# Kernel optimization log

Hardware: AMD Instinct MI355X
Metric: run time of the kernel (lower is better)

Reference implementation:

```python
import jax, jax.numpy as jnp
import numpy as np
from jax import lax

NPOINT = 1024
RADIUS = 0.2
NSAMPLE = 32
BN_EPS = 1e-5


def farthest_point_sample(xyz, npoint):
    # xyz: (B, N, 3). Deterministic start at index 0 (torch version starts at a
    # random index; the algorithm is otherwise identical).
    B, N, _ = xyz.shape

    def step(carry, _):
        distance, farthest = carry
        centroid = jnp.take_along_axis(xyz, farthest[:, None, None], axis=1)  # (B,1,3)
        d = jnp.sum((xyz - centroid) ** 2, axis=-1)  # (B,N)
        distance = jnp.minimum(distance, d)
        new_farthest = jnp.argmax(distance, axis=-1).astype(jnp.int32)
        return (distance, new_farthest), farthest

    init = (jnp.full((B, N), 1e10, xyz.dtype), jnp.zeros((B,), jnp.int32))
    _, centroids = lax.scan(step, init, None, length=npoint)  # (npoint, B)
    return centroids.T  # (B, npoint)


def batched_gather(points, idx):
    # points: (B, N, C); idx: (B, ...) -> (B, ..., C)
    return jax.vmap(lambda p, i: p[i])(points, idx)


def square_distance(src, dst):
    # src: (B,S,3), dst: (B,N,3) -> (B,S,N)
    d = -2.0 * jnp.einsum('bsc,bnc->bsn', src, dst)
    d += jnp.sum(src ** 2, -1)[:, :, None]
    d += jnp.sum(dst ** 2, -1)[:, None, :]
    return d


def query_ball_point(radius, nsample, xyz, new_xyz):
    B, N, _ = xyz.shape
    S = new_xyz.shape[1]
    sqrdists = square_distance(new_xyz, xyz)                 # (B,S,N)
    neg_d, idx = lax.top_k(-sqrdists, nsample)               # smallest nsample dists
    out_of_ball = (-neg_d) > radius ** 2                     # (B,S,nsample)
    first = idx[:, :, 0]
    # if even the nearest point is outside the ball, group the centroid itself
    first = jnp.where(out_of_ball[:, :, 0], jnp.arange(S, dtype=idx.dtype)[None, :], first)
    idx = jnp.where(out_of_ball, first[:, :, None], idx)
    return idx


def sa_forward(xyz_b3n, points_bdn, params):
    xyz = jnp.transpose(xyz_b3n, (0, 2, 1))      # (B,N,3)
    pts = jnp.transpose(points_bdn, (0, 2, 1))   # (B,N,D)
    fps_idx = farthest_point_sample(xyz, NPOINT)             # (B,S)
    new_xyz = batched_gather(xyz, fps_idx)                   # (B,S,3)
    idx = query_ball_point(RADIUS, NSAMPLE, xyz, new_xyz)    # (B,S,K)
    grouped_xyz = batched_gather(xyz, idx)                   # (B,S,K,3)
    grouped_xyz_norm = grouped_xyz - new_xyz[:, :, None, :]
    grouped_pts = batched_gather(pts, idx)                   # (B,S,K,D)
    x = jnp.concatenate([grouped_xyz_norm, grouped_pts], -1) # (B,S,K,3+D)

    for (w, b, gamma, beta) in params:
        x = jnp.einsum('bskc,oc->bsko', x, w) + b            # 1x1 conv
        mu = jnp.mean(x, axis=(0, 1, 2))
        var = jnp.var(x, axis=(0, 1, 2))                     # biased, as torch BN
        x = jax.nn.relu(gamma * (x - mu) * lax.rsqrt(var + BN_EPS) + beta)

    new_points = jnp.max(x, axis=2)                          # max over nsample K
    return (jnp.transpose(new_xyz, (0, 2, 1)),
            jnp.transpose(new_points, (0, 2, 1)),
            fps_idx)


def setup_inputs() -> dict:
    key = jax.random.key(0)
    ks = jax.random.split(key, 8)
    B, N, D = 16, 4096, 64
    xyz = jax.random.uniform(ks[0], (B, 3, N), dtype=jnp.float32)
    points = jax.random.normal(ks[1], (B, D, N), dtype=jnp.float32)
    mlp = [64, 64, 128]
    last = 3 + D  # in_channel = 67
    inp = {'xyz': xyz, 'points': points}
    for i, out in enumerate(mlp):
        inp[f'w{i}'] = jax.random.normal(ks[2 + i], (out, last), dtype=jnp.float32) * (1.0 / np.sqrt(last))
        inp[f'b{i}'] = jnp.zeros((out,), jnp.float32)
        inp[f'gamma{i}'] = jnp.ones((out,), jnp.float32)
        inp[f'beta{i}'] = jnp.zeros((out,), jnp.float32)
        last = out
    return inp


def reference(xyz, points, w0, b0, gamma0, beta0, w1, b1, gamma1, beta1, w2, b2, gamma2, beta2):
    params = [(w0, b0, gamma0, beta0), (w1, b1, gamma1, beta1), (w2, b2, gamma2, beta2)]
    return sa_forward(xyz, points, params)
```

## Files before the change

kernel.cpp:

```cpp
#include <hip/hip_runtime.h>

using f32x2  = __attribute__((ext_vector_type(2))) float;
using f32x4  = __attribute__((ext_vector_type(4))) float;
using short8 = __attribute__((ext_vector_type(8))) short;
using u64x2  = __attribute__((ext_vector_type(2))) unsigned long long;

__device__ __forceinline__ unsigned short f2bf(float f) {
  unsigned u = __builtin_bit_cast(unsigned, f);
  u = (u + 0x7FFFu + ((u >> 16) & 1u)) >> 16;
  return (unsigned short)u;
}
__device__ __forceinline__ float bf2f(unsigned short s) {
  return __builtin_bit_cast(float, ((unsigned)s) << 16);
}
__device__ __forceinline__ double u2d(unsigned long long u) {
  return __builtin_bit_cast(double, u);
}
__device__ __forceinline__ unsigned long long d2u(double d) {
  return __builtin_bit_cast(unsigned long long, d);
}
__device__ __forceinline__ unsigned cvt_pk_bf16(float lo, float hi) {
  unsigned r;
  asm("v_cvt_pk_bf16_f32 %0, %1, %2" : "=v"(r) : "v"(lo), "v"(hi));
  return r;
}

template <int CTRL>
__device__ __forceinline__ double dpp_max_f64(double best) {
  unsigned long long u = d2u(best);
  int lo32 = (int)(unsigned)u;
  int hi32 = (int)(unsigned)(u >> 32);
  int plo = __builtin_amdgcn_update_dpp(0, lo32, CTRL, 0xF, 0xF, true);
  int phi = __builtin_amdgcn_update_dpp(0, hi32, CTRL, 0xF, 0xF, true);
  unsigned long long p =
      ((unsigned long long)(unsigned)phi << 32) | (unsigned long long)(unsigned)plo;
  return fmax(best, u2d(p));
}
template <int CTRL>
__device__ __forceinline__ double dpp_min_f64(double v) {
  unsigned long long u = d2u(v);
  int lo32 = (int)(unsigned)u;
  int hi32 = (int)(unsigned)(u >> 32);
  int plo = __builtin_amdgcn_update_dpp(lo32, lo32, CTRL, 0xF, 0xF, false);
  int phi = __builtin_amdgcn_update_dpp(hi32, hi32, CTRL, 0xF, 0xF, false);
  unsigned long long p =
      ((unsigned long long)(unsigned)phi << 32) | (unsigned long long)(unsigned)plo;
  return fmin(v, u2d(p));
}

union SmemFP {
  struct {
    float4 sp4[4096];
    unsigned long long scand[2][16];
    int sfar[1024];
  } f;
  float tile[64][65];
};

__global__ __launch_bounds__(256, 1) void k_fp(const float* __restrict__ xyz,
                                               const float* __restrict__ points,
                                               float* __restrict__ out0,
                                               float* __restrict__ out2,
                                               int* __restrict__ fpsidx,
                                               float4* __restrict__ nq4,
                                               unsigned short* __restrict__ pT,
                                               float4* __restrict__ xyz4,
                                               const float* __restrict__ w0,
                                               const float* __restrict__ w1,
                                               const float* __restrict__ w2,
                                               unsigned short* __restrict__ wb0,
                                               unsigned short* __restrict__ wb1,
                                               unsigned short* __restrict__ wb2) {
  __shared__ SmemFP sm;
  int t = threadIdx.x, blk = blockIdx.x;
  if (blk >= 16) {
    int pb = blk - 16;
    if (pb == 1024) {
      for (int e = t; e < 64 * 96; e += 256) {
        int o = e / 96, k = e - o * 96;
        float v = (k < 64) ? w0[o * 67 + 3 + k] : ((k < 67) ? w0[o * 67 + (k - 64)] : 0.f);
        wb0[e] = f2bf(v);
      }
      for (int e = t; e < 4096; e += 256) wb1[e] = f2bf(w1[e]);
      for (int e = t; e < 8192; e += 256) wb2[e] = f2bf(w2[e]);
      return;
    }
    int b = pb >> 6, n0 = (pb & 63) << 6;
#pragma unroll
    for (int p = 0; p < 16; ++p) {
      int c = p * 4 + (t >> 6);
      sm.tile[c][t & 63] = points[(size_t)b * 262144 + (size_t)c * 4096 + n0 + (t & 63)];
    }
    if (t < 64) {
      int n = n0 + t;
      float x = xyz[(size_t)b * 12288 + n];
      float y = xyz[(size_t)b * 12288 + 4096 + n];
      float z = xyz[(size_t)b * 12288 + 8192 + n];
      float ps = __fadd_rn(__fadd_rn(__fmul_rn(x, x), __fmul_rn(y, y)), __fmul_rn(z, z));
      xyz4[(size_t)b * 4096 + n] = make_float4(x, y, z, ps);
    }
    __syncthreads();
    int nl = t >> 2, coff = (t & 3) * 16;
    unsigned v[8];
#pragma unroll
    for (int j = 0; j < 8; ++j)
      v[j] = cvt_pk_bf16(sm.tile[coff + 2 * j][nl], sm.tile[coff + 2 * j + 1][nl]);
    uint4* dst = reinterpret_cast<uint4*>(pT + ((size_t)b * 4096 + n0 + nl) * 64 + coff);
    dst[0] = make_uint4(v[0], v[1], v[2], v[3]);
    dst[1] = make_uint4(v[4], v[5], v[6], v[7]);
    return;
  }
  int b = blk;
  float px[16], py[16], pz[16], dist[16];
#pragma unroll
  for (int j = 0; j < 16; ++j) {
    int n = t + (j << 8);
    float x = xyz[(size_t)b * 12288 + n];
    float y = xyz[(size_t)b * 12288 + 4096 + n];
    float z = xyz[(size_t)b * 12288 + 8192 + n];
    px[j] = x; py[j] = y; pz[j] = z; dist[j] = 1e10f;
    sm.f.sp4[n] = make_float4(x, y, z, 0.f);
  }
  __syncthreads();
#pragma unroll
  for (int j = 0; j < 16; ++j) {
    asm volatile("" : "+v"(px[j]), "+v"(py[j]), "+v"(pz[j]));
  }
  unsigned nt = ~(unsigned)t;
  int far = 0;
  float cx = sm.f.sp4[0].x, cy = sm.f.sp4[0].y, cz = sm.f.sp4[0].z;
  for (int it = 0; it < 1024; ++it) {
    if (t == 0) sm.f.sfar[it] = far;
    double best0 = 0.0, best1 = 0.0;
#pragma unroll
    for (int j = 0; j < 16; ++j) {
      float dx = __fsub_rn(px[j], cx);
      float dy = __fsub_rn(py[j], cy);
      float dz = __fsub_rn(pz[j], cz);
      float d  = __fadd_rn(__fadd_rn(__fmul_rn(dx, dx), __fmul_rn(dy, dy)), __fmul_rn(dz, dz));
      float nd = fminf(dist[j], d);
      dist[j] = nd;
      unsigned long long cand =
          ((unsigned long long)__builtin_bit_cast(unsigned, nd) << 32) |
          (unsigned long long)(nt - (unsigned)(j << 8));
      if (j & 1) best1 = fmax(best1, u2d(cand));
      else       best0 = fmax(best0, u2d(cand));
    }
    double best = fmax(best0, best1);
    best = dpp_max_f64<0xB1>(best);
    best = dpp_max_f64<0x4E>(best);
    best = dpp_max_f64<0x124>(best);
    best = dpp_max_f64<0x128>(best);
    int pb = it & 1;
    if ((t & 15) == 0) sm.f.scand[pb][t >> 4] = d2u(best);
    __syncthreads();
    const u64x2* cp = reinterpret_cast<const u64x2*>(sm.f.scand[pb]);
    u64x2 q0 = cp[0], q1 = cp[1], q2 = cp[2], q3 = cp[3];
    u64x2 q4 = cp[4], q5 = cp[5], q6 = cp[6], q7 = cp[7];
    double a0 = fmax(u2d(q0[0]), u2d(q0[1]));
    double a1 = fmax(u2d(q1[0]), u2d(q1[1]));
    double a2 = fmax(u2d(q2[0]), u2d(q2[1]));
    double a3 = fmax(u2d(q3[0]), u2d(q3[1]));
    double a4 = fmax(u2d(q4[0]), u2d(q4[1]));
    double a5 = fmax(u2d(q5[0]), u2d(q5[1]));
    double a6 = fmax(u2d(q6[0]), u2d(q6[1]));
    double a7 = fmax(u2d(q7[0]), u2d(q7[1]));
    double b0 = fmax(fmax(a0, a1), fmax(a2, a3));
    double b1 = fmax(fmax(a4, a5), fmax(a6, a7));
    unsigned long long bw = d2u(fmax(b0, b1));
    int n = (int)(~(unsigned)bw) & 4095;
    far = n;
    float4 c4 = sm.f.sp4[n];
    cx = c4.x; cy = c4.y; cz = c4.z;
  }
  __syncthreads();
#pragma unroll
  for (int h = 0; h < 4; ++h) {
    int k = (h << 8) + t;
    int fr = sm.f.sfar[k];
    float4 p = sm.f.sp4[fr];
    float x = p.x, y = p.y, z = p.z;
    fpsidx[(b << 10) + k] = fr;
    out2[(b << 10) + k] = (float)fr;
    out0[(size_t)b * 3072 + k]        = x;
    out0[(size_t)b * 3072 + 1024 + k] = y;
    out0[(size_t)b * 3072 + 2048 + k] = z;
    float ps = __fadd_rn(__fadd_rn(__fmul_rn(x, x), __fmul_rn(y, y)), __fmul_rn(z, z));
    nq4[(b << 10) + k] = make_float4(x, y, z, ps);
  }
}

#define BCAP 384
__global__ __launch_bounds__(256) void k_ball(const float4* __restrict__ xyz4,
                                              const int* __restrict__ fpsidx,
                                              int* __restrict__ ballidx) {
  __shared__ __align__(16) float4 sp[4096];
  __shared__ unsigned long long spk[4][BCAP];
  const unsigned long long INVP = 0x7149F2CAFFFFFFFFull;
  int t = threadIdx.x, blk = blockIdx.x;
  int b = blk >> 6;
  for (int i = t; i < 4096; i += 256) sp[i] = xyz4[(size_t)b * 4096 + i];
  __syncthreads();
  int lane = t & 63, wid = t >> 6;
  for (int r = 0; r < 4; ++r) {
    int q = blk * 16 + r * 4 + wid;
    int qi = fpsidx[q];
    float4 Q = sp[qi];
    float qx = Q.x, qy = Q.y, qz = Q.z, qs = Q.w;
    int cnt = 0;
    for (int i = 0; i < 64; ++i) {
      int n = (i << 6) + lane;
      float4 P = sp[n];
      float dot = __fadd_rn(__fadd_rn(__fmul_rn(qx, P.x), __fmul_rn(qy, P.y)), __fmul_rn(qz, P.z));
      float d   = __fadd_rn(__fadd_rn(__fmul_rn(-2.f, dot), qs), P.w);
      bool in = (d <= 0.04f);
      unsigned long long m = __ballot(in);
      int pos = cnt + (int)__popcll(m & ((1ull << lane) - 1ull));
      if (in && pos < BCAP)
        spk[wid][pos] = ((unsigned long long)__builtin_bit_cast(unsigned, d) << 32) | (unsigned)n;
      cnt += (int)__popcll(m);
    }
    if (cnt > BCAP) cnt = BCAP;
    double c0, c1, c2, c3, c4, c5;
    {
      int s0 = lane, s1 = lane + 64, s2 = lane + 128, s3 = lane + 192, s4 = lane + 256, s5 = lane + 320;
      c0 = (s0 < cnt) ? u2d(spk[wid][s0]) : u2d(INVP);
      c1 = (s1 < cnt) ? u2d(spk[wid][s1]) : u2d(INVP);
      c2 = (s2 < cnt) ? u2d(spk[wid][s2]) : u2d(INVP);
      c3 = (s3 < cnt) ? u2d(spk[wid][s3]) : u2d(INVP);
      c4 = (s4 < cnt) ? u2d(spk[wid][s4]) : u2d(INVP);
      c5 = (s5 < cnt) ? u2d(spk[wid][s5]) : u2d(INVP);
    }
#define CE(a, b) { double mn_ = fmin(a, b), mx_ = fmax(a, b); a = mn_; b = mx_; }
    CE(c0, c1);
    CE(c1, c2); CE(c0, c1);
    CE(c2, c3); CE(c1, c2); CE(c0, c1);
    CE(c3, c4); CE(c2, c3); CE(c1, c2); CE(c0, c1);
    CE(c4, c5); CE(c3, c4); CE(c2, c3); CE(c1, c2); CE(c0, c1);
#undef CE
    int firstI = 0;
#pragma unroll 1
    for (int rr = 0; rr < 32; ++rr) {
      double h = c0;
      h = dpp_min_f64<0xB1>(h);
      h = dpp_min_f64<0x4E>(h);
      h = dpp_min_f64<0x124>(h);
      h = dpp_min_f64<0x128>(h);
      unsigned long long hu = d2u(h);
      int lo = (int)(unsigned)hu, hi = (int)(unsigned)(hu >> 32);
      unsigned long long r0 = ((unsigned long long)(unsigned)__builtin_amdgcn_readlane(hi, 0)  << 32) | (unsigned)__builtin_amdgcn_readlane(lo, 0);
      unsigned long long r1 = ((unsigned long long)(unsigned)__builtin_amdgcn_readlane(hi, 16) << 32) | (unsigned)__builtin_amdgcn_readlane(lo, 16);
      unsigned long long r2 = ((unsigned long long)(unsigned)__builtin_amdgcn_readlane(hi, 32) << 32) | (unsigned)__builtin_amdgcn_readlane(lo, 32);
      unsigned long long r3 = ((unsigned long long)(unsigned)__builtin_amdgcn_readlane(hi, 48) << 32) | (unsigned)__builtin_amdgcn_readlane(lo, 48);
      double w = fmin(fmin(u2d(r0), u2d(r1)), fmin(u2d(r2), u2d(r3)));
      unsigned long long wu = d2u(w);
      int wi = (int)(unsigned)wu;
      if (rr == 0) firstI = wi;
      int outv = (wu < INVP) ? wi : firstI;
      if (lane == 0) ballidx[(size_t)q * 32 + rr] = outv;
      if (d2u(c0) == wu) {
        c0 = c1; c1 = c2; c2 = c3; c3 = c4; c4 = c5; c5 = u2d(INVP);
      }
    }
  }
}

__global__ __launch_bounds__(256) void k_gemm1(const unsigned short* __restrict__ pT,
    const float4* __restrict__ xyz4, const float4* __restrict__ nq4,
    const int* __restrict__ bidx, const unsigned short* __restrict__ wb,
    const float* __restrict__ bia, unsigned short* __restrict__ xbuf,
    float* __restrict__ part) {
  __shared__ unsigned short A[64][104];
  __shared__ unsigned short W[64][104];
  __shared__ float sred[4][2][64];
  int t = threadIdx.x, blk = blockIdx.x;
  int b = blk >> 9;
  for (int e = t; e < 768; e += 256) {
    int o = e / 12, k8 = e - o * 12;
    *reinterpret_cast<uint4*>(&W[o][k8 * 8]) = reinterpret_cast<const uint4*>(wb)[e];
  }
  {
    int rt = t >> 2, sub = t & 3;
    int q = (blk << 1) + (rt >> 5);
    int n = bidx[(size_t)q * 32 + (rt & 31)];
    const uint4* src = reinterpret_cast<const uint4*>(pT + ((size_t)(b * 4096 + n)) * 64 + sub * 16);
    uint4 v0 = src[0], v1 = src[1];
    *reinterpret_cast<uint4*>(&A[rt][sub * 16])     = v0;
    *reinterpret_cast<uint4*>(&A[rt][sub * 16 + 8]) = v1;
    if (sub == 0) {
      float4 P = xyz4[(size_t)b * 4096 + n];
      float4 Qc = nq4[q];
      A[rt][64] = f2bf(__fsub_rn(P.x, Qc.x));
      A[rt][65] = f2bf(__fsub_rn(P.y, Qc.y));
      A[rt][66] = f2bf(__fsub_rn(P.z, Qc.z));
    } else if (sub == 1) {
#pragma unroll
      for (int k = 67; k < 96; ++k) A[rt][k] = 0;
    }
  }
  __syncthreads();
  int lane = t & 63, wid = t >> 6;
  int cl = lane & 15, rg = lane >> 4;
  int rowb = (wid << 4) + cl, ko = rg << 3;
  f32x4 acc[4] = {};
#pragma unroll
  for (int ks = 0; ks < 96; ks += 32) {
    short8 a = *reinterpret_cast<const short8*>(&A[rowb][ks + ko]);
#pragma unroll
    for (int nt = 0; nt < 4; ++nt) {
      short8 bb = *reinterpret_cast<const short8*>(&W[nt * 16 + cl][ks + ko]);
      acc[nt] = __builtin_amdgcn_mfma_f32_16x16x32_bf16(a, bb, acc[nt], 0, 0, 0);
    }
  }
#pragma unroll
  for (int nt = 0; nt < 4; ++nt) {
    int ch = nt * 16 + cl;
    float bv = bia[ch];
    float v0 = acc[nt][0] + bv, v1 = acc[nt][1] + bv, v2 = acc[nt][2] + bv, v3 = acc[nt][3] + bv;
    size_t gr = (size_t)blk * 64 + (wid << 4) + (rg << 2);
    xbuf[(gr + 0) * 64 + ch] = f2bf(v0);
    xbuf[(gr + 1) * 64 + ch] = f2bf(v1);
    xbuf[(gr + 2) * 64 + ch] = f2bf(v2);
    xbuf[(gr + 3) * 64 + ch] = f2bf(v3);
    float s1 = (v0 + v1) + (v2 + v3);
    float s2 = (v0 * v0 + v1 * v1) + (v2 * v2 + v3 * v3);
    s1 += __shfl_xor(s1, 16); s1 += __shfl_xor(s1, 32);
    s2 += __shfl_xor(s2, 16); s2 += __shfl_xor(s2, 32);
    if (rg == 0) { sred[wid][0][ch] = s1; sred[wid][1][ch] = s2; }
  }
  __syncthreads();
  if (t < 128) {
    int ch = t & 63, wh = t >> 6;
    float v = sred[0][wh][ch] + sred[1][wh][ch] + sred[2][wh][ch] + sred[3][wh][ch];
    part[(size_t)blk * 128 + ch * 2 + wh] = v;
  }
}

__global__ __launch_bounds__(256) void k_red(const float* __restrict__ part, int nblk, int nch,
    const float* __restrict__ gamma, const float* __restrict__ beta,
    float* __restrict__ scale, float* __restrict__ shift) {
  int c = blockIdx.x, t = threadIdx.x;
  int stride = 2 * nch;
  float s1 = 0.f, s2 = 0.f;
  for (int i = t; i < nblk; i += 256) {
    s1 += part[(size_t)i * stride + 2 * c];
    s2 += part[(size_t)i * stride + 2 * c + 1];
  }
  __shared__ float r1[256], r2[256];
  r1[t] = s1; r2[t] = s2;
  __syncthreads();
  for (int o = 128; o > 0; o >>= 1) {
    if (t < o) { r1[t] += r1[t + o]; r2[t] += r2[t + o]; }
    __syncthreads();
  }
  if (t == 0) {
    const float N = 524288.f;
    float mu = r1[0] / N;
    float var = r2[0] / N - mu * mu;
    float a = gamma[c] / sqrtf(var + 1e-5f);
    scale[c] = a;
    shift[c] = beta[c] - a * mu;
  }
}

__global__ __launch_bounds__(256) void k_gemm2(unsigned short* __restrict__ xbuf,
    const unsigned short* __restrict__ wb, const float* __restrict__ bia,
    const float* __restrict__ sc, const float* __restrict__ sh,
    float* __restrict__ part) {
  __shared__ unsigned short A[64][72];
  __shared__ unsigned short W[64][72];
  __shared__ float ssc[64], ssh[64];
  __shared__ float sred[4][2][64];
  int t = threadIdx.x, blk = blockIdx.x;
  if (t < 64) { ssc[t] = sc[t]; ssh[t] = sh[t]; }
  __syncthreads();
  for (int e = t; e < 512; e += 256) {
    int o = e >> 3, k8 = e & 7;
    *reinterpret_cast<uint4*>(&W[o][k8 * 8]) = reinterpret_cast<const uint4*>(wb)[e];
  }
  {
    int rt = t >> 2, sub = t & 3;
    size_t gr = (size_t)blk * 64 + rt;
    const uint4* src = reinterpret_cast<const uint4*>(xbuf + gr * 64 + sub * 16);
    uint4 v0 = src[0], v1 = src[1];
    unsigned wv[8] = {v0.x, v0.y, v0.z, v0.w, v1.x, v1.y, v1.z, v1.w};
    unsigned pk[8];
#pragma unroll
    for (int j = 0; j < 8; ++j) {
      int c = sub * 16 + 2 * j;
      float x0 = bf2f((unsigned short)(wv[j] & 0xffffu));
      float x1 = bf2f((unsigned short)(wv[j] >> 16));
      float a0 = fmaxf(0.f, ssc[c] * x0 + ssh[c]);
      float a1 = fmaxf(0.f, ssc[c + 1] * x1 + ssh[c + 1]);
      pk[j] = cvt_pk_bf16(a0, a1);
    }
    *reinterpret_cast<uint4*>(&A[rt][sub * 16])     = make_uint4(pk[0], pk[1], pk[2], pk[3]);
    *reinterpret_cast<uint4*>(&A[rt][sub * 16 + 8]) = make_uint4(pk[4], pk[5], pk[6], pk[7]);
  }
  __syncthreads();
  int lane = t & 63, wid = t >> 6;
  int cl = lane & 15, rg = lane >> 4;
  int rowb = (wid << 4) + cl, ko = rg << 3;
  f32x4 acc[4] = {};
#pragma unroll
  for (int ks = 0; ks < 64; ks += 32) {
    short8 a = *reinterpret_cast<const short8*>(&A[rowb][ks + ko]);
#pragma unroll
    for (int nt = 0; nt < 4; ++nt) {
      short8 bb = *reinterpret_cast<const short8*>(&W[nt * 16 + cl][ks + ko]);
      acc[nt] = __builtin_amdgcn_mfma_f32_16x16x32_bf16(a, bb, acc[nt], 0, 0, 0);
    }
  }
#pragma unroll
  for (int nt = 0; nt < 4; ++nt) {
    int ch = nt * 16 + cl;
    float bv = bia[ch];
    float v0 = acc[nt][0] + bv, v1 = acc[nt][1] + bv, v2 = acc[nt][2] + bv, v3 = acc[nt][3] + bv;
    size_t gr = (size_t)blk * 64 + (wid << 4) + (rg << 2);
    xbuf[(gr + 0) * 64 + ch] = f2bf(v0);
    xbuf[(gr + 1) * 64 + ch] = f2bf(v1);
    xbuf[(gr + 2) * 64 + ch] = f2bf(v2);
    xbuf[(gr + 3) * 64 + ch] = f2bf(v3);
    float s1 = (v0 + v1) + (v2 + v3);
    float s2 = (v0 * v0 + v1 * v1) + (v2 * v2 + v3 * v3);
    s1 += __shfl_xor(s1, 16); s1 += __shfl_xor(s1, 32);
    s2 += __shfl_xor(s2, 16); s2 += __shfl_xor(s2, 32);
    if (rg == 0) { sred[wid][0][ch] = s1; sred[wid][1][ch] = s2; }
  }
  __syncthreads();
  if (t < 128) {
    int ch = t & 63, wh = t >> 6;
    float v = sred[0][wh][ch] + sred[1][wh][ch] + sred[2][wh][ch] + sred[3][wh][ch];
    part[(size_t)blk * 128 + ch * 2 + wh] = v;
  }
}

__global__ __launch_bounds__(256) void k_gemm3(unsigned short* xbuf,
    const unsigned short* __restrict__ wb, const float* __restrict__ bia,
    const float* __restrict__ sc2, const float* __restrict__ sh2,
    float* __restrict__ part) {
  __shared__ unsigned short A[64][72];
  __shared__ unsigned short W[128][72];
  __shared__ float ssc[64], ssh[64];
  __shared__ float sred[4][4][128];
  int t = threadIdx.x, blk = blockIdx.x;
  if (t < 64) { ssc[t] = sc2[t]; ssh[t] = sh2[t]; }
  __syncthreads();
  for (int e = t; e < 1024; e += 256) {
    int o = e >> 3, k8 = e & 7;
    *reinterpret_cast<uint4*>(&W[o][k8 * 8]) = reinterpret_cast<const uint4*>(wb)[e];
  }
  {
    int rt = t >> 2, sub = t & 3;
    size_t gr = (size_t)blk * 64 + rt;
    const uint4* src = reinterpret_cast<const uint4*>(xbuf + gr * 64 + sub * 16);
    uint4 v0 = src[0], v1 = src[1];
    unsigned wv[8] = {v0.x, v0.y, v0.z, v0.w, v1.x, v1.y, v1.z, v1.w};
    unsigned pk[8];
#pragma unroll
    for (int j = 0; j < 8; ++j) {
      int c = sub * 16 + 2 * j;
      float x0 = bf2f((unsigned short)(wv[j] & 0xffffu));
      float x1 = bf2f((unsigned short)(wv[j] >> 16));
      float a0 = fmaxf(0.f, ssc[c] * x0 + ssh[c]);
      float a1 = fmaxf(0.f, ssc[c + 1] * x1 + ssh[c + 1]);
      pk[j] = cvt_pk_bf16(a0, a1);
    }
    *reinterpret_cast<uint4*>(&A[rt][sub * 16])     = make_uint4(pk[0], pk[1], pk[2], pk[3]);
    *reinterpret_cast<uint4*>(&A[rt][sub * 16 + 8]) = make_uint4(pk[4], pk[5], pk[6], pk[7]);
  }
  __syncthreads();
  int lane = t & 63, wid = t >> 6;
  int cl = lane & 15, rg = lane >> 4;
  int rowb = (wid << 4) + cl, ko = rg << 3;
  f32x4 acc[8] = {};
#pragma unroll
  for (int ks = 0; ks < 64; ks += 32) {
    short8 a = *reinterpret_cast<const short8*>(&A[rowb][ks + ko]);
#pragma unroll
    for (int nt = 0; nt < 8; ++nt) {
      short8 bb = *reinterpret_cast<const short8*>(&W[nt * 16 + cl][ks + ko]);
      acc[nt] = __builtin_amdgcn_mfma_f32_16x16x32_bf16(a, bb, acc[nt], 0, 0, 0);
    }
  }
#pragma unroll
  for (int nt = 0; nt < 8; ++nt) {
    int ch = nt * 16 + cl;
    float bv = bia[ch];
    float v0 = acc[nt][0] + bv, v1 = acc[nt][1] + bv, v2 = acc[nt][2] + bv, v3 = acc[nt][3] + bv;
    float s1 = (v0 + v1) + (v2 + v3);
    float s2 = (v0 * v0 + v1 * v1) + (v2 * v2 + v3 * v3);
    float mx = fmaxf(fmaxf(v0, v1), fmaxf(v2, v3));
    float mn = fminf(fminf(v0, v1), fminf(v2, v3));
    s1 += __shfl_xor(s1, 16); s1 += __shfl_xor(s1, 32);
    s2 += __shfl_xor(s2, 16); s2 += __shfl_xor(s2, 32);
    mx = fmaxf(mx, __shfl_xor(mx, 16)); mx = fmaxf(mx, __shfl_xor(mx, 32));
    mn = fminf(mn, __shfl_xor(mn, 16)); mn = fminf(mn, __shfl_xor(mn, 32));
    if (rg == 0) {
      sred[wid][0][ch] = s1; sred[wid][1][ch] = s2;
      sred[wid][2][ch] = mx; sred[wid][3][ch] = mn;
    }
  }
  __syncthreads();
  {
    int ch = t & 127, wh = t >> 7;
    part[(size_t)blk * 256 + ch * 2 + wh] =
        sred[0][wh][ch] + sred[1][wh][ch] + sred[2][wh][ch] + sred[3][wh][ch];
    float mx = fmaxf(sred[2 * wh][2][ch], sred[2 * wh + 1][2][ch]);
    float mn = fminf(sred[2 * wh][3][ch], sred[2 * wh + 1][3][ch]);
    float* mm = reinterpret_cast<float*>(xbuf) + (size_t)blk * 2048;
    mm[wh * 256 + ch]       = mx;
    mm[wh * 256 + 128 + ch] = mn;
  }
}

__global__ __launch_bounds__(256) void k_fin(const float* __restrict__ mm,
                                             const float* __restrict__ sc3,
                                             const float* __restrict__ sh3,
                                             float* __restrict__ out1) {
  __shared__ float tile[32][33];
  int t = threadIdx.x, blk = blockIdx.x;
  int b = blk >> 7, rem = blk & 127, ct = rem >> 5, st = rem & 31;
  int c0 = ct * 32, s0 = st * 32;
#pragma unroll
  for (int p = 0; p < 4; ++p) {
    int s_local = (t >> 5) + p * 8;
    int c = c0 + (t & 31);
    int q = (b << 10) + s0 + s_local;
    size_t base = (size_t)(q >> 1) * 2048 + (size_t)(q & 1) * 256;
    float mx = mm[base + c];
    float mn = mm[base + 128 + c];
    float sc = sc3[c], sh = sh3[c];
    float v = (sc >= 0.f) ? mx : mn;
    tile[t & 31][s_local] = fmaxf(0.f, sc * v + sh);
  }
  __syncthreads();
#pragma unroll
  for (int p = 0; p < 4; ++p) {
    int c = c0 + (t >> 5) + p * 8;
    int s = s0 + (t & 31);
    out1[(size_t)b * 131072 + (size_t)c * 1024 + s] = tile[(t >> 5) + p * 8][t & 31];
  }
}

extern "C" void kernel_launch(void* const* d_in, const int* in_sizes, int n_in,
                              void* d_out, int out_size, void* d_ws, size_t ws_size,
                              hipStream_t stream) {
  (void)in_sizes; (void)n_in; (void)out_size;
  const float* xyz    = (const float*)d_in[0];
  const float* points = (const float*)d_in[1];
  const float* w0  = (const float*)d_in[2];
  const float* b0  = (const float*)d_in[3];
  const float* g0  = (const float*)d_in[4];
  const float* be0 = (const float*)d_in[5];
  const float* w1  = (const float*)d_in[6];
  const float* b1  = (const float*)d_in[7];
  const float* g1  = (const float*)d_in[8];
  const float* be1 = (const float*)d_in[9];
  const float* w2  = (const float*)d_in[10];
  const float* b2  = (const float*)d_in[11];
  const float* g2  = (const float*)d_in[12];
  const float* be2 = (const float*)d_in[13];
  float* out  = (float*)d_out;
  float* out0 = out;
  float* out1 = out + 49152;
  float* out2 = out + 49152 + 2097152;
  char* ws = (char*)d_ws;
  const size_t OFF_PT    = 0;
  const size_t OFF_XYZ4  = 8388608;
  const size_t OFF_NQ4   = 9437184;
  const size_t OFF_FPS   = 9699328;
  const size_t OFF_BALL  = 9764864;
  const size_t OFF_XBUF  = 11862016;
  const size_t OFF_PART  = 78970880;
  const size_t OFF_SC    = 87359488;
  const size_t OFF_WB    = 87363584;
  const size_t NEED      = 87400448;
  if (ws_size < NEED) return;
  unsigned short* pT   = (unsigned short*)(ws + OFF_PT);
  float4* xyz4 = (float4*)(ws + OFF_XYZ4);
  float4* nq4  = (float4*)(ws + OFF_NQ4);
  int* fpsidx  = (int*)(ws + OFF_FPS);
  int* ballidx = (int*)(ws + OFF_BALL);
  unsigned short* xbuf = (unsigned short*)(ws + OFF_XBUF);
  float* part  = (float*)(ws + OFF_PART);
  float* scb   = (float*)(ws + OFF_SC);
  float *sc1 = scb, *sh1 = scb + 128, *sc2 = scb + 256, *sh2 = scb + 384,
        *sc3 = scb + 512, *sh3 = scb + 640;
  unsigned short* wb0 = (unsigned short*)(ws + OFF_WB);
  unsigned short* wb1 = wb0 + 6144;
  unsigned short* wb2 = wb1 + 4096;

  k_fp<<<1041, 256, 0, stream>>>(xyz, points, out0, out2, fpsidx, nq4,
                                 pT, xyz4, w0, w1, w2, wb0, wb1, wb2);
  k_ball<<<1024, 256, 0, stream>>>(xyz4, fpsidx, ballidx);
  k_gemm1<<<8192, 256, 0, stream>>>(pT, xyz4, nq4, ballidx, wb0, b0, xbuf, part);
  k_red<<<64, 256, 0, stream>>>(part, 8192, 64, g0, be0, sc1, sh1);
  k_gemm2<<<8192, 256, 0, stream>>>(xbuf, wb1, b1, sc1, sh1, part);
  k_red<<<64, 256, 0, stream>>>(part, 8192, 64, g1, be1, sc2, sh2);
  k_gemm3<<<8192, 256, 0, stream>>>(xbuf, wb2, b2, sc2, sh2, part);
  k_red<<<128, 256, 0, stream>>>(part, 8192, 128, g2, be2, sc3, sh3);
  k_fin<<<2048, 256, 0, stream>>>((const float*)xbuf, sc3, sh3, out1);
}
```

Before: 851.9 us.

## Fuse FPS, ball query and first GEMM into a persistent cooperative megakernel

Merges the farthest-point-sampling, data prep, ball-query and first-layer GEMM kernels into a single persistent cooperative kernel. The FPS blocks publish sampled centroids incrementally through progress flags, so ball-query and GEMM work can begin on finished centroids while FPS is still running. The goal is to hide the long serial FPS loop behind the downstream stages and to remove kernel launch boundaries. In exchange it adds spin-wait synchronisation, a flag memset and an occupancy query on every call, and it depends on all blocks being co-resident.

```diff
diff --git a/kernel.cpp b/kernel.cpp
--- a/kernel.cpp
+++ b/kernel.cpp
@@ -1,6 +1,5 @@
 #include <hip/hip_runtime.h>
 
-using f32x2  = __attribute__((ext_vector_type(2))) float;
 using f32x4  = __attribute__((ext_vector_type(4))) float;
 using short8 = __attribute__((ext_vector_type(8))) short;
 using u64x2  = __attribute__((ext_vector_type(2))) unsigned long long;
@@ -48,188 +47,104 @@
   return fmin(v, u2d(p));
 }
 
-union SmemFP {
-  struct {
-    float4 sp4[4096];
-    unsigned long long scand[2][16];
-    int sfar[1024];
-  } f;
+#define BCAP 384
+
+union __align__(16) SmemMega {
+  struct { float4 sp4[4096]; unsigned long long scand[2][16]; int sfar[1024]; } f;
   float tile[64][65];
+  struct { float4 sp[4096]; unsigned long long spk[4][BCAP]; } bq;
+  struct { unsigned short A[64][104]; unsigned short W[64][104]; float sred[4][2][64]; } g1;
 };
 
-__global__ __launch_bounds__(256, 1) void k_fp(const float* __restrict__ xyz,
-                                               const float* __restrict__ points,
-                                               float* __restrict__ out0,
-                                               float* __restrict__ out2,
-                                               int* __restrict__ fpsidx,
-                                               float4* __restrict__ nq4,
-                                               unsigned short* __restrict__ pT,
-                                               float4* __restrict__ xyz4,
-                                               const float* __restrict__ w0,
-                                               const float* __restrict__ w1,
-                                               const float* __restrict__ w2,
-                                               unsigned short* __restrict__ wb0,
-                                               unsigned short* __restrict__ wb1,
-                                               unsigned short* __restrict__ wb2) {
-  __shared__ SmemFP sm;
-  int t = threadIdx.x, blk = blockIdx.x;
-  if (blk >= 16) {
-    int pb = blk - 16;
-    if (pb == 1024) {
-      for (int e = t; e < 64 * 96; e += 256) {
-        int o = e / 96, k = e - o * 96;
-        float v = (k < 64) ? w0[o * 67 + 3 + k] : ((k < 67) ? w0[o * 67 + (k - 64)] : 0.f);
-        wb0[e] = f2bf(v);
-      }
-      for (int e = t; e < 4096; e += 256) wb1[e] = f2bf(w1[e]);
-      for (int e = t; e < 8192; e += 256) wb2[e] = f2bf(w2[e]);
-      return;
-    }
-    int b = pb >> 6, n0 = (pb & 63) << 6;
-#pragma unroll
-    for (int p = 0; p < 16; ++p) {
-      int c = p * 4 + (t >> 6);
-      sm.tile[c][t & 63] = points[(size_t)b * 262144 + (size_t)c * 4096 + n0 + (t & 63)];
-    }
-    if (t < 64) {
-      int n = n0 + t;
-      float x = xyz[(size_t)b * 12288 + n];
-      float y = xyz[(size_t)b * 12288 + 4096 + n];
-      float z = xyz[(size_t)b * 12288 + 8192 + n];
-      float ps = __fadd_rn(__fadd_rn(__fmul_rn(x, x), __fmul_rn(y, y)), __fmul_rn(z, z));
-      xyz4[(size_t)b * 4096 + n] = make_float4(x, y, z, ps);
-    }
-    __syncthreads();
-    int nl = t >> 2, coff = (t & 3) * 16;
-    unsigned v[8];
-#pragma unroll
-    for (int j = 0; j < 8; ++j)
-      v[j] = cvt_pk_bf16(sm.tile[coff + 2 * j][nl], sm.tile[coff + 2 * j + 1][nl]);
-    uint4* dst = reinterpret_cast<uint4*>(pT + ((size_t)b * 4096 + n0 + nl) * 64 + coff);
-    dst[0] = make_uint4(v[0], v[1], v[2], v[3]);
-    dst[1] = make_uint4(v[4], v[5], v[6], v[7]);
-    return;
-  }
-  int b = blk;
-  float px[16], py[16], pz[16], dist[16];
-#pragma unroll
-  for (int j = 0; j < 16; ++j) {
-    int n = t + (j << 8);
-    float x = xyz[(size_t)b * 12288 + n];
-    float y = xyz[(size_t)b * 12288 + 4096 + n];
-    float z = xyz[(size_t)b * 12288 + 8192 + n];
-    px[j] = x; py[j] = y; pz[j] = z; dist[j] = 1e10f;
-    sm.f.sp4[n] = make_float4(x, y, z, 0.f);
-  }
-  __syncthreads();
-#pragma unroll
-  for (int j = 0; j < 16; ++j) {
-    asm volatile("" : "+v"(px[j]), "+v"(py[j]), "+v"(pz[j]));
-  }
-  unsigned nt = ~(unsigned)t;
-  int far = 0;
-  float cx = sm.f.sp4[0].x, cy = sm.f.sp4[0].y, cz = sm.f.sp4[0].z;
-  for (int it = 0; it < 1024; ++it) {
-    if (t == 0) sm.f.sfar[it] = far;
-    double best0 = 0.0, best1 = 0.0;
-#pragma unroll
-    for (int j = 0; j < 16; ++j) {
-      float dx = __fsub_rn(px[j], cx);
-      float dy = __fsub_rn(py[j], cy);
-      float dz = __fsub_rn(pz[j], cz);
-      float d  = __fadd_rn(__fadd_rn(__fmul_rn(dx, dx), __fmul_rn(dy, dy)), __fmul_rn(dz, dz));
-      float nd = fminf(dist[j], d);
-      dist[j] = nd;
-      unsigned long long cand =
-          ((unsigned long long)__builtin_bit_cast(unsigned, nd) << 32) |
-          (unsigned long long)(nt - (unsigned)(j << 8));
-      if (j & 1) best1 = fmax(best1, u2d(cand));
-      else       best0 = fmax(best0, u2d(cand));
-    }
-    double best = fmax(best0, best1);
-    best = dpp_max_f64<0xB1>(best);
-    best = dpp_max_f64<0x4E>(best);
-    best = dpp_max_f64<0x124>(best);
-    best = dpp_max_f64<0x128>(best);
-    int pb = it & 1;
-    if ((t & 15) == 0) sm.f.scand[pb][t >> 4] = d2u(best);
-    __syncthreads();
-    const u64x2* cp = reinterpret_cast<const u64x2*>(sm.f.scand[pb]);
-    u64x2 q0 = cp[0], q1 = cp[1], q2 = cp[2], q3 = cp[3];
-    u64x2 q4 = cp[4], q5 = cp[5], q6 = cp[6], q7 = cp[7];
-    double a0 = fmax(u2d(q0[0]), u2d(q0[1]));
-    double a1 = fmax(u2d(q1[0]), u2d(q1[1]));
-    double a2 = fmax(u2d(q2[0]), u2d(q2[1]));
-    double a3 = fmax(u2d(q3[0]), u2d(q3[1]));
-    double a4 = fmax(u2d(q4[0]), u2d(q4[1]));
-    double a5 = fmax(u2d(q5[0]), u2d(q5[1]));
-    double a6 = fmax(u2d(q6[0]), u2d(q6[1]));
-    double a7 = fmax(u2d(q7[0]), u2d(q7[1]));
-    double b0 = fmax(fmax(a0, a1), fmax(a2, a3));
-    double b1 = fmax(fmax(a4, a5), fmax(a6, a7));
-    unsigned long long bw = d2u(fmax(b0, b1));
-    int n = (int)(~(unsigned)bw) & 4095;
-    far = n;
-    float4 c4 = sm.f.sp4[n];
-    cx = c4.x; cy = c4.y; cz = c4.z;
-  }
-  __syncthreads();
-#pragma unroll
-  for (int h = 0; h < 4; ++h) {
-    int k = (h << 8) + t;
-    int fr = sm.f.sfar[k];
-    float4 p = sm.f.sp4[fr];
-    float x = p.x, y = p.y, z = p.z;
-    fpsidx[(b << 10) + k] = fr;
-    out2[(b << 10) + k] = (float)fr;
-    out0[(size_t)b * 3072 + k]        = x;
-    out0[(size_t)b * 3072 + 1024 + k] = y;
-    out0[(size_t)b * 3072 + 2048 + k] = z;
+struct MegaP {
+  const float* xyz; const float* points;
+  float* out0; float* out2;
+  int* fpsidx; float4* nq4;
+  unsigned short* pT; float4* xyz4;
+  const float* w0; const float* w1; const float* w2;
+  unsigned short* wb0; unsigned short* wb1; unsigned short* wb2;
+  const float* b0;
+  unsigned short* xbuf; float* part;
+  int* bidx;
+  int* prog; int* prepcnt; int* wflag; int* ballprog;
+  int nc;
+};
+
+__device__ __forceinline__ void fps_publish(const MegaP& P, SmemMega& sm, int b, int k) {
+  int fr = sm.f.sfar[k];
+  float4 p = sm.f.sp4[fr];
+  P.fpsidx[(b << 10) + k] = fr;
+  P.out2[(b << 10) + k] = (float)fr;
+  P.out0[(size_t)b * 3072 + k]        = p.x;
+  P.out0[(size_t)b * 3072 + 1024 + k] = p.y;
+  P.out0[(size_t)b * 3072 + 2048 + k] = p.z;
+  float ps = __fadd_rn(__fadd_rn(__fmul_rn(p.x, p.x), __fmul_rn(p.y, p.y)), __fmul_rn(p.z, p.z));
+  P.nq4[(b << 10) + k] = make_float4(p.x, p.y, p.z, ps);
+}
+
+__device__ __forceinline__ void do_prep(int pb, SmemMega& sm, const MegaP& P) {
+  int t = threadIdx.x;
+  int b = pb >> 6, n0 = (pb & 63) << 6;
+#pragma unroll
+  for (int p = 0; p < 16; ++p) {
+    int c = p * 4 + (t >> 6);
+    sm.tile[c][t & 63] = P.points[(size_t)b * 262144 + (size_t)c * 4096 + n0 + (t & 63)];
+  }
+  if (t < 64) {
+    int n = n0 + t;
+    float x = P.xyz[(size_t)b * 12288 + n];
+    float y = P.xyz[(size_t)b * 12288 + 4096 + n];
+    float z = P.xyz[(size_t)b * 12288 + 8192 + n];
     float ps = __fadd_rn(__fadd_rn(__fmul_rn(x, x), __fmul_rn(y, y)), __fmul_rn(z, z));
-    nq4[(b << 10) + k] = make_float4(x, y, z, ps);
-  }
-}
-
-#define BCAP 384
-__global__ __launch_bounds__(256) void k_ball(const float4* __restrict__ xyz4,
-                                              const int* __restrict__ fpsidx,
-                                              int* __restrict__ ballidx) {
-  __shared__ __align__(16) float4 sp[4096];
-  __shared__ unsigned long long spk[4][BCAP];
+    P.xyz4[(size_t)b * 4096 + n] = make_float4(x, y, z, ps);
+  }
+  __syncthreads();
+  int nl = t >> 2, coff = (t & 3) * 16;
+  unsigned v[8];
+#pragma unroll
+  for (int j = 0; j < 8; ++j)
+    v[j] = cvt_pk_bf16(sm.tile[coff + 2 * j][nl], sm.tile[coff + 2 * j + 1][nl]);
+  uint4* dst = reinterpret_cast<uint4*>(P.pT + ((size_t)b * 4096 + n0 + nl) * 64 + coff);
+  dst[0] = make_uint4(v[0], v[1], v[2], v[3]);
+  dst[1] = make_uint4(v[4], v[5], v[6], v[7]);
+  __syncthreads();
+}
+
+__device__ __forceinline__ void do_ball(int w, SmemMega& sm, const MegaP& P) {
   const unsigned long long INVP = 0x7149F2CAFFFFFFFFull;
-  int t = threadIdx.x, blk = blockIdx.x;
-  int b = blk >> 6;
-  for (int i = t; i < 4096; i += 256) sp[i] = xyz4[(size_t)b * 4096 + i];
+  int t = threadIdx.x;
+  int b = w >> 6;
+  for (int i = t; i < 4096; i += 256) sm.bq.sp[i] = P.xyz4[(size_t)b * 4096 + i];
   __syncthreads();
   int lane = t & 63, wid = t >> 6;
   for (int r = 0; r < 4; ++r) {
-    int q = blk * 16 + r * 4 + wid;
-    int qi = fpsidx[q];
-    float4 Q = sp[qi];
+    int q = w * 16 + r * 4 + wid;
+    int qi = P.fpsidx[q];
+    float4 Q = sm.bq.sp[qi];
     float qx = Q.x, qy = Q.y, qz = Q.z, qs = Q.w;
     int cnt = 0;
     for (int i = 0; i < 64; ++i) {
       int n = (i << 6) + lane;
-      float4 P = sp[n];
-      float dot = __fadd_rn(__fadd_rn(__fmul_rn(qx, P.x), __fmul_rn(qy, P.y)), __fmul_rn(qz, P.z));
-      float d   = __fadd_rn(__fadd_rn(__fmul_rn(-2.f, dot), qs), P.w);
+      float4 Pp = sm.bq.sp[n];
+      float dot = __fadd_rn(__fadd_rn(__fmul_rn(qx, Pp.x), __fmul_rn(qy, Pp.y)), __fmul_rn(qz, Pp.z));
+      float d   = __fadd_rn(__fadd_rn(__fmul_rn(-2.f, dot), qs), Pp.w);
       bool in = (d <= 0.04f);
       unsigned long long m = __ballot(in);
       int pos = cnt + (int)__popcll(m & ((1ull << lane) - 1ull));
       if (in && pos < BCAP)
-        spk[wid][pos] = ((unsigned long long)__builtin_bit_cast(unsigned, d) << 32) | (unsigned)n;
+        sm.bq.spk[wid][pos] = ((unsigned long long)__builtin_bit_cast(unsigned, d) << 32) | (unsigned)n;
       cnt += (int)__popcll(m);
     }
     if (cnt > BCAP) cnt = BCAP;
     double c0, c1, c2, c3, c4, c5;
     {
       int s0 = lane, s1 = lane + 64, s2 = lane + 128, s3 = lane + 192, s4 = lane + 256, s5 = lane + 320;
-      c0 = (s0 < cnt) ? u2d(spk[wid][s0]) : u2d(INVP);
-      c1 = (s1 < cnt) ? u2d(spk[wid][s1]) : u2d(INVP);
-      c2 = (s2 < cnt) ? u2d(spk[wid][s2]) : u2d(INVP);
-      c3 = (s3 < cnt) ? u2d(spk[wid][s3]) : u2d(INVP);
-      c4 = (s4 < cnt) ? u2d(spk[wid][s4]) : u2d(INVP);
-      c5 = (s5 < cnt) ? u2d(spk[wid][s5]) : u2d(INVP);
+      c0 = (s0 < cnt) ? u2d(sm.bq.spk[wid][s0]) : u2d(INVP);
+      c1 = (s1 < cnt) ? u2d(sm.bq.spk[wid][s1]) : u2d(INVP);
+      c2 = (s2 < cnt) ? u2d(sm.bq.spk[wid][s2]) : u2d(INVP);
+      c3 = (s3 < cnt) ? u2d(sm.bq.spk[wid][s3]) : u2d(INVP);
+      c4 = (s4 < cnt) ? u2d(sm.bq.spk[wid][s4]) : u2d(INVP);
+      c5 = (s5 < cnt) ? u2d(sm.bq.spk[wid][s5]) : u2d(INVP);
     }
 #define CE(a, b) { double mn_ = fmin(a, b), mx_ = fmax(a, b); a = mn_; b = mx_; }
     CE(c0, c1);
@@ -252,50 +167,42 @@
       unsigned long long r1 = ((unsigned long long)(unsigned)__builtin_amdgcn_readlane(hi, 16) << 32) | (unsigned)__builtin_amdgcn_readlane(lo, 16);
       unsigned long long r2 = ((unsigned long long)(unsigned)__builtin_amdgcn_readlane(hi, 32) << 32) | (unsigned)__builtin_amdgcn_readlane(lo, 32);
       unsigned long long r3 = ((unsigned long long)(unsigned)__builtin_amdgcn_readlane(hi, 48) << 32) | (unsigned)__builtin_amdgcn_readlane(lo, 48);
-      double w = fmin(fmin(u2d(r0), u2d(r1)), fmin(u2d(r2), u2d(r3)));
-      unsigned long long wu = d2u(w);
+      double ww = fmin(fmin(u2d(r0), u2d(r1)), fmin(u2d(r2), u2d(r3)));
+      unsigned long long wu = d2u(ww);
       int wi = (int)(unsigned)wu;
       if (rr == 0) firstI = wi;
       int outv = (wu < INVP) ? wi : firstI;
-      if (lane == 0) ballidx[(size_t)q * 32 + rr] = outv;
-      if (d2u(c0) == wu) {
-        c0 = c1; c1 = c2; c2 = c3; c3 = c4; c4 = c5; c5 = u2d(INVP);
-      }
-    }
-  }
-}
-
-__global__ __launch_bounds__(256) void k_gemm1(const unsigned short* __restrict__ pT,
-    const float4* __restrict__ xyz4, const float4* __restrict__ nq4,
-    const int* __restrict__ bidx, const unsigned short* __restrict__ wb,
-    const float* __restrict__ bia, unsigned short* __restrict__ xbuf,
-    float* __restrict__ part) {
-  __shared__ unsigned short A[64][104];
-  __shared__ unsigned short W[64][104];
-  __shared__ float sred[4][2][64];
-  int t = threadIdx.x, blk = blockIdx.x;
-  int b = blk >> 9;
+      if (lane == 0) P.bidx[(size_t)q * 32 + rr] = outv;
+      if (d2u(c0) == wu) { c0 = c1; c1 = c2; c2 = c3; c3 = c4; c4 = c5; c5 = u2d(INVP); }
+    }
+  }
+  __syncthreads();
+}
+
+__device__ __forceinline__ void do_gemm1(int w, SmemMega& sm, const MegaP& P) {
+  int t = threadIdx.x;
+  int b = w >> 9;
   for (int e = t; e < 768; e += 256) {
     int o = e / 12, k8 = e - o * 12;
-    *reinterpret_cast<uint4*>(&W[o][k8 * 8]) = reinterpret_cast<const uint4*>(wb)[e];
+    *reinterpret_cast<uint4*>(&sm.g1.W[o][k8 * 8]) = reinterpret_cast<const uint4*>(P.wb0)[e];
   }
   {
     int rt = t >> 2, sub = t & 3;
-    int q = (blk << 1) + (rt >> 5);
-    int n = bidx[(size_t)q * 32 + (rt & 31)];
-    const uint4* src = reinterpret_cast<const uint4*>(pT + ((size_t)(b * 4096 + n)) * 64 + sub * 16);
+    int q = (w << 1) + (rt >> 5);
+    int n = P.bidx[(size_t)q * 32 + (rt & 31)];
+    const uint4* src = reinterpret_cast<const uint4*>(P.pT + ((size_t)(b * 4096 + n)) * 64 + sub * 16);
     uint4 v0 = src[0], v1 = src[1];
-    *reinterpret_cast<uint4*>(&A[rt][sub * 16])     = v0;
-    *reinterpret_cast<uint4*>(&A[rt][sub * 16 + 8]) = v1;
+    *reinterpret_cast<uint4*>(&sm.g1.A[rt][sub * 16])     = v0;
+    *reinterpret_cast<uint4*>(&sm.g1.A[rt][sub * 16 + 8]) = v1;
     if (sub == 0) {
-      float4 P = xyz4[(size_t)b * 4096 + n];
-      float4 Qc = nq4[q];
-      A[rt][64] = f2bf(__fsub_rn(P.x, Qc.x));
-      A[rt][65] = f2bf(__fsub_rn(P.y, Qc.y));
-      A[rt][66] = f2bf(__fsub_rn(P.z, Qc.z));
+      float4 Pt = P.xyz4[(size_t)b * 4096 + n];
+      float4 Qc = P.nq4[q];
+      sm.g1.A[rt][64] = f2bf(__fsub_rn(Pt.x, Qc.x));
+      sm.g1.A[rt][65] = f2bf(__fsub_rn(Pt.y, Qc.y));
+      sm.g1.A[rt][66] = f2bf(__fsub_rn(Pt.z, Qc.z));
     } else if (sub == 1) {
 #pragma unroll
-      for (int k = 67; k < 96; ++k) A[rt][k] = 0;
+      for (int k = 67; k < 96; ++k) sm.g1.A[rt][k] = 0;
     }
   }
   __syncthreads();
@@ -305,34 +212,151 @@
   f32x4 acc[4] = {};
 #pragma unroll
   for (int ks = 0; ks < 96; ks += 32) {
-    short8 a = *reinterpret_cast<const short8*>(&A[rowb][ks + ko]);
+    short8 a = *reinterpret_cast<const short8*>(&sm.g1.A[rowb][ks + ko]);
 #pragma unroll
     for (int nt = 0; nt < 4; ++nt) {
-      short8 bb = *reinterpret_cast<const short8*>(&W[nt * 16 + cl][ks + ko]);
+      short8 bb = *reinterpret_cast<const short8*>(&sm.g1.W[nt * 16 + cl][ks + ko]);
       acc[nt] = __builtin_amdgcn_mfma_f32_16x16x32_bf16(a, bb, acc[nt], 0, 0, 0);
     }
   }
 #pragma unroll
   for (int nt = 0; nt < 4; ++nt) {
     int ch = nt * 16 + cl;
-    float bv = bia[ch];
+    float bv = P.b0[ch];
     float v0 = acc[nt][0] + bv, v1 = acc[nt][1] + bv, v2 = acc[nt][2] + bv, v3 = acc[nt][3] + bv;
-    size_t gr = (size_t)blk * 64 + (wid << 4) + (rg << 2);
-    xbuf[(gr + 0) * 64 + ch] = f2bf(v0);
-    xbuf[(gr + 1) * 64 + ch] = f2bf(v1);
-    xbuf[(gr + 2) * 64 + ch] = f2bf(v2);
-    xbuf[(gr + 3) * 64 + ch] = f2bf(v3);
+    size_t gr = (size_t)w * 64 + (wid << 4) + (rg << 2);
+    P.xbuf[(gr + 0) * 64 + ch] = f2bf(v0);
+    P.xbuf[(gr + 1) * 64 + ch] = f2bf(v1);
+    P.xbuf[(gr + 2) * 64 + ch] = f2bf(v2);
+    P.xbuf[(gr + 3) * 64 + ch] = f2bf(v3);
     float s1 = (v0 + v1) + (v2 + v3);
     float s2 = (v0 * v0 + v1 * v1) + (v2 * v2 + v3 * v3);
     s1 += __shfl_xor(s1, 16); s1 += __shfl_xor(s1, 32);
     s2 += __shfl_xor(s2, 16); s2 += __shfl_xor(s2, 32);
-    if (rg == 0) { sred[wid][0][ch] = s1; sred[wid][1][ch] = s2; }
+    if (rg == 0) { sm.g1.sred[wid][0][ch] = s1; sm.g1.sred[wid][1][ch] = s2; }
   }
   __syncthreads();
   if (t < 128) {
     int ch = t & 63, wh = t >> 6;
-    float v = sred[0][wh][ch] + sred[1][wh][ch] + sred[2][wh][ch] + sred[3][wh][ch];
-    part[(size_t)blk * 128 + ch * 2 + wh] = v;
+    float v = sm.g1.sred[0][wh][ch] + sm.g1.sred[1][wh][ch] + sm.g1.sred[2][wh][ch] + sm.g1.sred[3][wh][ch];
+    P.part[(size_t)w * 128 + ch * 2 + wh] = v;
+  }
+  __syncthreads();
+}
+
+__global__ __launch_bounds__(256) void k_mega(MegaP P) {
+  __shared__ SmemMega sm;
+  int t = threadIdx.x, blk = blockIdx.x;
+  if (blk < 16) {
+    __builtin_amdgcn_s_setprio(2);
+    int b = blk;
+    float px[16], py[16], pz[16], dist[16];
+#pragma unroll
+    for (int j = 0; j < 16; ++j) {
+      int n = t + (j << 8);
+      float x = P.xyz[(size_t)b * 12288 + n];
+      float y = P.xyz[(size_t)b * 12288 + 4096 + n];
+      float z = P.xyz[(size_t)b * 12288 + 8192 + n];
+      px[j] = x; py[j] = y; pz[j] = z; dist[j] = 1e10f;
+      sm.f.sp4[n] = make_float4(x, y, z, 0.f);
+    }
+    __syncthreads();
+#pragma unroll
+    for (int j = 0; j < 16; ++j) {
+      asm volatile("" : "+v"(px[j]), "+v"(py[j]), "+v"(pz[j]));
+    }
+    unsigned nt = ~(unsigned)t;
+    int far = 0;
+    float cx = sm.f.sp4[0].x, cy = sm.f.sp4[0].y, cz = sm.f.sp4[0].z;
+    for (int it = 0; it < 1024; ++it) {
+      if (t == 0) sm.f.sfar[it] = far;
+      if ((it & 15) == 0 && it != 0 && t < 16) fps_publish(P, sm, b, it - 16 + t);
+      double best0 = 0.0, best1 = 0.0;
+#pragma unroll
+      for (int j = 0; j < 16; ++j) {
+        float dx = __fsub_rn(px[j], cx);
+        float dy = __fsub_rn(py[j], cy);
+        float dz = __fsub_rn(pz[j], cz);
+        float d  = __fadd_rn(__fadd_rn(__fmul_rn(dx, dx), __fmul_rn(dy, dy)), __fmul_rn(dz, dz));
+        float nd = fminf(dist[j], d);
+        dist[j] = nd;
+        unsigned long long cand =
+            ((unsigned long long)__builtin_bit_cast(unsigned, nd) << 32) |
+            (unsigned long long)(nt - (unsigned)(j << 8));
+        if (j & 1) best1 = fmax(best1, u2d(cand));
+        else       best0 = fmax(best0, u2d(cand));
+      }
+      double best = fmax(best0, best1);
+      best = dpp_max_f64<0xB1>(best);
+      best = dpp_max_f64<0x4E>(best);
+      best = dpp_max_f64<0x124>(best);
+      best = dpp_max_f64<0x128>(best);
+      int pb = it & 1;
+      if ((t & 15) == 0) sm.f.scand[pb][t >> 4] = d2u(best);
+      __syncthreads();
+      if ((it & 15) == 0 && it != 0 && t == 0) { __threadfence(); atomicExch(&P.prog[b], it); }
+      const u64x2* cp = reinterpret_cast<const u64x2*>(sm.f.scand[pb]);
+      u64x2 q0 = cp[0], q1 = cp[1], q2 = cp[2], q3 = cp[3];
+      u64x2 q4 = cp[4], q5 = cp[5], q6 = cp[6], q7 = cp[7];
+      double a0 = fmax(u2d(q0[0]), u2d(q0[1]));
+      double a1 = fmax(u2d(q1[0]), u2d(q1[1]));
+      double a2 = fmax(u2d(q2[0]), u2d(q2[1]));
+      double a3 = fmax(u2d(q3[0]), u2d(q3[1]));
+      double a4 = fmax(u2d(q4[0]), u2d(q4[1]));
+      double a5 = fmax(u2d(q5[0]), u2d(q5[1]));
+      double a6 = fmax(u2d(q6[0]), u2d(q6[1]));
+      double a7 = fmax(u2d(q7[0]), u2d(q7[1]));
+      double b0 = fmax(fmax(a0, a1), fmax(a2, a3));
+      double b1 = fmax(fmax(a4, a5), fmax(a6, a7));
+      unsigned long long bw = d2u(fmax(b0, b1));
+      int n = (int)(~(unsigned)bw) & 4095;
+      far = n;
+      float4 c4 = sm.f.sp4[n];
+      cx = c4.x; cy = c4.y; cz = c4.z;
+    }
+    __syncthreads();
+    if (t < 16) fps_publish(P, sm, b, 1008 + t);
+    __syncthreads();
+    if (t == 0) { __threadfence(); atomicExch(&P.prog[b], 1024); }
+    return;
+  }
+  int ci = blk - 16, NC = P.nc;
+  for (int w = ci; w < 1025; w += NC) {
+    if (w == 1024) {
+      for (int e = t; e < 64 * 96; e += 256) {
+        int o = e / 96, k = e - o * 96;
+        float v = (k < 64) ? P.w0[o * 67 + 3 + k] : ((k < 67) ? P.w0[o * 67 + (k - 64)] : 0.f);
+        P.wb0[e] = f2bf(v);
+      }
+      for (int e = t; e < 4096; e += 256) P.wb1[e] = f2bf(P.w1[e]);
+      for (int e = t; e < 8192; e += 256) P.wb2[e] = f2bf(P.w2[e]);
+      __syncthreads();
+      if (t == 0) { __threadfence(); atomicExch(P.wflag, 1); }
+    } else {
+      do_prep(w, sm, P);
+      if (t == 0) { __threadfence(); atomicAdd(&P.prepcnt[w >> 6], 1); }
+    }
+  }
+  for (int w = ci; w < 1024; w += NC) {
+    int b = w >> 6, need = ((w & 63) + 1) << 4;
+    if (t == 0) {
+      while (atomicAdd(&P.prepcnt[b], 0) < 64) __builtin_amdgcn_s_sleep(16);
+      while (atomicAdd(&P.prog[b], 0) < need) __builtin_amdgcn_s_sleep(16);
+      __threadfence();
+    }
+    __syncthreads();
+    do_ball(w, sm, P);
+    if (t == 0) { __threadfence(); atomicExch(&P.ballprog[w], 1); }
+  }
+  for (int w = ci; w < 8192; w += NC) {
+    int idx = ((w >> 9) << 6) + ((w & 511) >> 3);
+    if (t == 0) {
+      while (atomicAdd(P.wflag, 0) < 1) __builtin_amdgcn_s_sleep(16);
+      while (atomicAdd(&P.ballprog[idx], 0) < 1) __builtin_amdgcn_s_sleep(16);
+      __threadfence();
+    }
+    __syncthreads();
+    do_gemm1(w, sm, P);
   }
 }
 
@@ -575,7 +599,8 @@
   const size_t OFF_PART  = 78970880;
   const size_t OFF_SC    = 87359488;
   const size_t OFF_WB    = 87363584;
-  const size_t NEED      = 87400448;
+  const size_t OFF_FLAGS = 87400448;
+  const size_t NEED      = 87408640;
   if (ws_size < NEED) return;
   unsigned short* pT   = (unsigned short*)(ws + OFF_PT);
   float4* xyz4 = (float4*)(ws + OFF_XYZ4);
@@ -590,11 +615,35 @@
   unsigned short* wb0 = (unsigned short*)(ws + OFF_WB);
   unsigned short* wb1 = wb0 + 6144;
   unsigned short* wb2 = wb1 + 4096;
-
-  k_fp<<<1041, 256, 0, stream>>>(xyz, points, out0, out2, fpsidx, nq4,
-                                 pT, xyz4, w0, w1, w2, wb0, wb1, wb2);
-  k_ball<<<1024, 256, 0, stream>>>(xyz4, fpsidx, ballidx);
-  k_gemm1<<<8192, 256, 0, stream>>>(pT, xyz4, nq4, ballidx, wb0, b0, xbuf, part);
+  int* flags = (int*)(ws + OFF_FLAGS);
+  int* prog = flags;
+  int* prepcnt = flags + 16;
+  int* wflag = flags + 32;
+  int* ballprog = flags + 64;
+
+  hipMemsetAsync(ws + OFF_FLAGS, 0, 8192, stream);
+
+  int nb = 0;
+  hipOccupancyMaxActiveBlocksPerMultiprocessor(&nb, reinterpret_cast<const void*>(k_mega), 256, 0);
+  int G = nb * 256;
+  if (G > 512) G = 512;
+  if (G < 32) G = 32;
+
+  MegaP P;
+  P.xyz = xyz; P.points = points;
+  P.out0 = out0; P.out2 = out2;
+  P.fpsidx = fpsidx; P.nq4 = nq4;
+  P.pT = pT; P.xyz4 = xyz4;
+  P.w0 = w0; P.w1 = w1; P.w2 = w2;
+  P.wb0 = wb0; P.wb1 = wb1; P.wb2 = wb2;
+  P.b0 = b0;
+  P.xbuf = xbuf; P.part = part;
+  P.bidx = ballidx;
+  P.prog = prog; P.prepcnt = prepcnt; P.wflag = wflag; P.ballprog = ballprog;
+  P.nc = G - 16;
+  void* args[] = { &P };
+  hipLaunchCooperativeKernel(reinterpret_cast<void*>(k_mega), dim3(G), dim3(256), args, 0, stream);
+
   k_red<<<64, 256, 0, stream>>>(part, 8192, 64, g0, be0, sc1, sh1);
   k_gemm2<<<8192, 256, 0, stream>>>(xbuf, wb1, b1, sc1, sh1, part);
   k_red<<<64, 256, 0, stream>>>(part, 8192, 64, g1, be1, sc2, sh2);
```

Result: slower. 1.208 ms (+41.9%).
